# Kernel tuning notes

Measured on AMD Instinct MI355X. Metric: run time of the kernel, lower is better.

The kernel has to match this reference:

```python
import jax, jax.numpy as jnp
import numpy as np

B, T, D, H = 8, 4096, 1024, 1024


def log_g(x):
    # log of g(x) = relu(x)+0.5 for x>=0, sigmoid(x) for x<0 (continuous at 0)
    return jnp.where(x >= 0, jnp.log(jax.nn.relu(x) + 0.5), -jax.nn.softplus(-x))


def setup_inputs() -> dict:
    key = jax.random.key(0)
    k0, k1, k2, k3, k4, k5 = jax.random.split(key, 6)
    s = 1.0 / np.sqrt(D)
    return {
        "x": jax.random.normal(k0, (B, T, D), jnp.float32),
        "h_0": jax.random.normal(k1, (B, H), jnp.float32),
        "Wz": jax.random.uniform(k2, (H, D), jnp.float32, -s, s),
        "bz": jax.random.uniform(k3, (H,), jnp.float32, -s, s),
        "Wh": jax.random.uniform(k4, (H, D), jnp.float32, -s, s),
        "bh": jax.random.uniform(k5, (H,), jnp.float32, -s, s),
    }


def reference(x, h_0, Wz, bz, Wh, bh):
    # gate pre-activation k: (B,T,H)
    k = jnp.einsum("btd,hd->bth", x, Wz) + bz
    log_z = -jax.nn.softplus(-k)        # log sigmoid(k)
    log_coeffs = -jax.nn.softplus(k)    # log (1 - sigmoid(k))
    log_h_0 = log_g(h_0)[:, None, :]    # (B,1,H)
    log_tilde_h = log_g(jnp.einsum("btd,hd->bth", x, Wh) + bh)
    log_values = jnp.concatenate([log_h_0, log_z + log_tilde_h], axis=1)  # (B,T+1,H)
    # parallel scan in log space
    a_star = jnp.pad(jnp.cumsum(log_coeffs, axis=1), ((0, 0), (1, 0), (0, 0)))
    log_h = a_star + jax.lax.cumlogsumexp(log_values - a_star, axis=1)
    h = jnp.exp(log_h)                  # (B,T+1,H)
    return h[:, -T:, :]
```

## Files before the change

kernel.cpp:

```cpp
#include <hip/hip_runtime.h>
#include <hip/hip_bf16.h>

#define Bb 8
#define Tt 4096
#define Dd 1024
#define Hh 1024
#define Mm (Bb * Tt)
#define NCHUNK 32
#define CLEN 128

typedef float f32x4 __attribute__((ext_vector_type(4)));
typedef short bf16x8 __attribute__((ext_vector_type(8)));

__device__ __forceinline__ unsigned f2bfu(float x) {
  unsigned u = __float_as_uint(x);
  return (u + 0x7fffu + ((u >> 16) & 1u)) >> 16;
}
__device__ __forceinline__ float bflo(unsigned u) { return __uint_as_float(u << 16); }
__device__ __forceinline__ float bfhi(unsigned u) { return __uint_as_float(u & 0xffff0000u); }

__global__ void cvt_kernel(const float* __restrict__ src, unsigned short* __restrict__ dst,
                           int n4) {
  int i = blockIdx.x * blockDim.x + threadIdx.x;
  int stride = gridDim.x * blockDim.x;
  for (; i < n4; i += stride) {
    float4 v = reinterpret_cast<const float4*>(src)[i];
    ushort4 o;
    o.x = (unsigned short)f2bfu(v.x);
    o.y = (unsigned short)f2bfu(v.y);
    o.z = (unsigned short)f2bfu(v.z);
    o.w = (unsigned short)f2bfu(v.w);
    reinterpret_cast<ushort4*>(dst)[i] = o;
  }
}

__device__ __forceinline__ void async16(const unsigned short* g, unsigned short* l) {
  __builtin_amdgcn_global_load_lds(
      (const __attribute__((address_space(1))) unsigned int*)g,
      (__attribute__((address_space(3))) unsigned int*)l, 16, 0, 0);
}

__global__ void __launch_bounds__(256, 2) gemm_kernel(
    const unsigned short* __restrict__ xb,
    const unsigned short* __restrict__ wzb,
    const unsigned short* __restrict__ whb,
    const float* __restrict__ bz,
    const float* __restrict__ bh,
    unsigned int* __restrict__ P) {
  __shared__ unsigned short As[128 * 64];
  __shared__ unsigned short Bs[128 * 64];
  const int m0 = blockIdx.x * 128;
  const int h0 = blockIdx.y * 64;
  const int t = threadIdx.x;
  const int w = t >> 6;
  const int l = t & 63;
  const int ln = l & 15;
  const int l4 = l >> 4;

  f32x4 acc[2][8];
#pragma unroll
  for (int mf = 0; mf < 2; ++mf)
#pragma unroll
    for (int nf = 0; nf < 8; ++nf)
      acc[mf][nf] = f32x4{0.f, 0.f, 0.f, 0.f};

  for (int kt = 0; kt < Dd / 64; ++kt) {
    const int k0 = kt * 64;
#pragma unroll
    for (int i = 0; i < 4; ++i) {
      const int blk = i * 256 + t;
      const int r = blk >> 3;
      const int slot = (blk & 7) ^ (r & 7);
      async16(xb + (size_t)(m0 + r) * Dd + (k0 + slot * 8), &As[blk * 8]);
    }
#pragma unroll
    for (int i = 0; i < 4; ++i) {
      const int blk = i * 256 + t;
      const int r = blk >> 3;
      const int slot = (blk & 7) ^ (r & 7);
      const unsigned short* src =
          (r < 64) ? (wzb + (size_t)(h0 + r) * Dd + (k0 + slot * 8))
                   : (whb + (size_t)(h0 + r - 64) * Dd + (k0 + slot * 8));
      async16(src, &Bs[blk * 8]);
    }
    __syncthreads();

#pragma unroll
    for (int kk = 0; kk < 2; ++kk) {
      bf16x8 af[2];
#pragma unroll
      for (int mf = 0; mf < 2; ++mf) {
        const int row = w * 32 + mf * 16 + ln;
        const int kb = (kk * 64 + l4 * 16) ^ ((row & 7) << 4);
        af[mf] = *reinterpret_cast<const bf16x8*>(
            reinterpret_cast<const char*>(As) + row * 128 + kb);
      }
#pragma unroll
      for (int nf = 0; nf < 8; ++nf) {
        const int row = nf * 16 + ln;
        const int kb = (kk * 64 + l4 * 16) ^ ((row & 7) << 4);
        bf16x8 bfr = *reinterpret_cast<const bf16x8*>(
            reinterpret_cast<const char*>(Bs) + row * 128 + kb);
#pragma unroll
        for (int mf = 0; mf < 2; ++mf)
          acc[mf][nf] =
              __builtin_amdgcn_mfma_f32_16x16x32_bf16(af[mf], bfr, acc[mf][nf], 0, 0, 0);
      }
    }
    __syncthreads();
  }

#pragma unroll
  for (int mf = 0; mf < 2; ++mf) {
#pragma unroll
    for (int nf = 0; nf < 4; ++nf) {
      const int hcol = h0 + nf * 16 + ln;
      const float bzv = bz[hcol];
      const float bhv = bh[hcol];
#pragma unroll
      for (int q = 0; q < 4; ++q) {
        const int m = m0 + w * 32 + mf * 16 + l4 * 4 + q;
        const float kv = acc[mf][nf][q] + bzv;
        const float pv = acc[mf][nf + 4][q] + bhv;
        const float ek = __expf(kv);
        const float a = 1.f / (1.f + ek);
        const float z = 1.f - a;
        const float g = (pv >= 0.f) ? (pv + 0.5f) : (1.f / (1.f + __expf(-pv)));
        const float c = z * g;
        P[(size_t)m * Hh + hcol] = f2bfu(a) | (f2bfu(c) << 16);
      }
    }
  }
}

__global__ void scan_pass1(const unsigned int* __restrict__ P,
                           float* __restrict__ Pp, float* __restrict__ Qq) {
  const int h = blockIdx.x * 256 + threadIdx.x;
  const int ch = blockIdx.y;
  const int b = blockIdx.z;
  const unsigned int* p = P + ((size_t)(b * Tt + ch * CLEN)) * Hh + h;
  float A = 1.f, Q = 0.f;
#pragma unroll 8
  for (int i = 0; i < CLEN; ++i) {
    const unsigned u = p[(size_t)i * Hh];
    Q = fmaf(bflo(u), Q, bfhi(u));
    A *= bflo(u);
  }
  const int idx = ch * (Bb * Hh) + b * Hh + h;
  Pp[idx] = A;
  Qq[idx] = Q;
}

__global__ void scan_pass2(const float* __restrict__ h0raw,
                           const float* __restrict__ Pp, const float* __restrict__ Qq,
                           float* __restrict__ Hinit) {
  const int bh = blockIdx.x * 256 + threadIdx.x;
  const float x = h0raw[bh];
  float hs = (x >= 0.f) ? (x + 0.5f) : (1.f / (1.f + __expf(-x)));
  for (int ch = 0; ch < NCHUNK; ++ch) {
    const int idx = ch * (Bb * Hh) + bh;
    Hinit[idx] = hs;
    hs = fmaf(Pp[idx], hs, Qq[idx]);
  }
}

__global__ void scan_pass3(const unsigned int* __restrict__ P,
                           const float* __restrict__ Hinit,
                           float* __restrict__ out) {
  const int h = blockIdx.x * 256 + threadIdx.x;
  const int ch = blockIdx.y;
  const int b = blockIdx.z;
  float hs = Hinit[ch * (Bb * Hh) + b * Hh + h];
  const size_t base = ((size_t)(b * Tt + ch * CLEN)) * Hh + h;
  const unsigned int* p = P + base;
  float* o = out + base;
#pragma unroll 8
  for (int i = 0; i < CLEN; ++i) {
    const unsigned u = p[(size_t)i * Hh];
    hs = fmaf(bflo(u), hs, bfhi(u));
    o[(size_t)i * Hh] = hs;
  }
}

extern "C" void kernel_launch(void* const* d_in, const int* in_sizes, int n_in,
                              void* d_out, int out_size, void* d_ws, size_t ws_size,
                              hipStream_t stream) {
  const float* x  = (const float*)d_in[0];
  const float* h0 = (const float*)d_in[1];
  const float* Wz = (const float*)d_in[2];
  const float* bz = (const float*)d_in[3];
  const float* Wh = (const float*)d_in[4];
  const float* bh = (const float*)d_in[5];
  float* out = (float*)d_out;

  char* ws = (char*)d_ws;
  unsigned short* xb  = (unsigned short*)(ws);
  unsigned short* wzb = (unsigned short*)(ws + 67108864);
  unsigned short* whb = (unsigned short*)(ws + 69206016);
  unsigned int*   P   = (unsigned int*)(ws + 71303168);
  float* Pp    = (float*)(ws + 205520896);
  float* Qq    = (float*)(ws + 206569472);
  float* Hinit = (float*)(ws + 207618048);

  cvt_kernel<<<4096, 256, 0, stream>>>(x, xb, Mm * Dd / 4);
  cvt_kernel<<<1024, 256, 0, stream>>>(Wz, wzb, Hh * Dd / 4);
  cvt_kernel<<<1024, 256, 0, stream>>>(Wh, whb, Hh * Dd / 4);

  dim3 ggrid(Mm / 128, Hh / 64);
  gemm_kernel<<<ggrid, 256, 0, stream>>>(xb, wzb, whb, bz, bh, P);

  dim3 sgrid(Hh / 256, NCHUNK, Bb);
  scan_pass1<<<sgrid, 256, 0, stream>>>(P, Pp, Qq);
  scan_pass2<<<Bb * Hh / 256, 256, 0, stream>>>(h0, Pp, Qq, Hinit);
  scan_pass3<<<sgrid, 256, 0, stream>>>(P, Hinit, out);
}
```

Measured before the change: 280.5 us.

## Rewrite GEMM as 256x128 tile with double-buffered async LDS pipeline

Replaces the 128x64 single-buffered GEMM with a 512-thread, 256x(64 Wz + 64 Wh interleaved) tile kernel. Global-to-LDS loads are double-buffered across K steps and interleaved with MFMA phases, using explicit vmcnt waits, barriers and setprio. It also adds a block-ID swizzle for L2 locality and a rotated LDS layout to avoid bank conflicts. The aim is to hide load latency and raise MFMA utilisation, at the cost of higher register and LDS pressure (128KB LDS, one block per CU) and hand-tuned synchronisation that could be fragile.

New measurement: 273.0 us. 2.7% less time.

```diff
diff --git a/kernel.cpp b/kernel.cpp
--- a/kernel.cpp
+++ b/kernel.cpp
@@ -40,88 +40,202 @@
       (__attribute__((address_space(3))) unsigned int*)l, 16, 0, 0);
 }
 
-__global__ void __launch_bounds__(256, 2) gemm_kernel(
+template <int MF0>
+__device__ __forceinline__ void mfma16(const bf16x8 af[4], const bf16x8 bfr[4],
+                                       f32x4 (&acc)[8][4]) {
+#pragma unroll
+  for (int i = 0; i < 4; ++i)
+#pragma unroll
+    for (int j = 0; j < 4; ++j)
+      acc[MF0 + i][j] =
+          __builtin_amdgcn_mfma_f32_16x16x32_bf16(af[i], bfr[j], acc[MF0 + i][j], 0, 0, 0);
+}
+
+__device__ __forceinline__ void phase_pre(bool guard) {
+  if (guard) asm volatile("s_waitcnt vmcnt(6)" ::: "memory");
+  __builtin_amdgcn_sched_barrier(0);
+  __builtin_amdgcn_s_barrier();
+}
+__device__ __forceinline__ void phase_post() {
+  __builtin_amdgcn_sched_barrier(0);
+  __builtin_amdgcn_s_barrier();
+}
+
+__global__ void __launch_bounds__(512, 1) gemm_kernel(
     const unsigned short* __restrict__ xb,
     const unsigned short* __restrict__ wzb,
     const unsigned short* __restrict__ whb,
     const float* __restrict__ bz,
     const float* __restrict__ bh,
     unsigned int* __restrict__ P) {
-  __shared__ unsigned short As[128 * 64];
-  __shared__ unsigned short Bs[128 * 64];
-  const int m0 = blockIdx.x * 128;
-  const int h0 = blockIdx.y * 64;
-  const int t = threadIdx.x;
-  const int w = t >> 6;
-  const int l = t & 63;
-  const int ln = l & 15;
-  const int l4 = l >> 4;
-
-  f32x4 acc[2][8];
-#pragma unroll
-  for (int mf = 0; mf < 2; ++mf)
-#pragma unroll
-    for (int nf = 0; nf < 8; ++nf)
-      acc[mf][nf] = f32x4{0.f, 0.f, 0.f, 0.f};
-
-  for (int kt = 0; kt < Dd / 64; ++kt) {
-    const int k0 = kt * 64;
-#pragma unroll
-    for (int i = 0; i < 4; ++i) {
-      const int blk = i * 256 + t;
-      const int r = blk >> 3;
-      const int slot = (blk & 7) ^ (r & 7);
-      async16(xb + (size_t)(m0 + r) * Dd + (k0 + slot * 8), &As[blk * 8]);
-    }
-#pragma unroll
-    for (int i = 0; i < 4; ++i) {
-      const int blk = i * 256 + t;
-      const int r = blk >> 3;
-      const int slot = (blk & 7) ^ (r & 7);
-      const unsigned short* src =
-          (r < 64) ? (wzb + (size_t)(h0 + r) * Dd + (k0 + slot * 8))
-                   : (whb + (size_t)(h0 + r - 64) * Dd + (k0 + slot * 8));
-      async16(src, &Bs[blk * 8]);
-    }
-    __syncthreads();
-
-#pragma unroll
-    for (int kk = 0; kk < 2; ++kk) {
-      bf16x8 af[2];
-#pragma unroll
-      for (int mf = 0; mf < 2; ++mf) {
-        const int row = w * 32 + mf * 16 + ln;
-        const int kb = (kk * 64 + l4 * 16) ^ ((row & 7) << 4);
-        af[mf] = *reinterpret_cast<const bf16x8*>(
-            reinterpret_cast<const char*>(As) + row * 128 + kb);
-      }
-#pragma unroll
-      for (int nf = 0; nf < 8; ++nf) {
-        const int row = nf * 16 + ln;
-        const int kb = (kk * 64 + l4 * 16) ^ ((row & 7) << 4);
-        bf16x8 bfr = *reinterpret_cast<const bf16x8*>(
-            reinterpret_cast<const char*>(Bs) + row * 128 + kb);
-#pragma unroll
-        for (int mf = 0; mf < 2; ++mf)
-          acc[mf][nf] =
-              __builtin_amdgcn_mfma_f32_16x16x32_bf16(af[mf], bfr, acc[mf][nf], 0, 0, 0);
-      }
-    }
-    __syncthreads();
-  }
-
-#pragma unroll
-  for (int mf = 0; mf < 2; ++mf) {
-#pragma unroll
-    for (int nf = 0; nf < 4; ++nf) {
-      const int hcol = h0 + nf * 16 + ln;
-      const float bzv = bz[hcol];
-      const float bhv = bh[hcol];
+  __shared__ unsigned short lds[65536];
+  const int tid = threadIdx.x;
+  const int wid = tid >> 6;
+  const int wm = wid >> 2;
+  const int wn = wid & 3;
+  const int l = tid & 63, ln = l & 15, l4 = l >> 4;
+
+  const int id = blockIdx.x;
+  const int sw = (id & 7) * 128 + (id >> 3);
+  const int mb = sw >> 3, nb = sw & 7;
+  const int m0 = mb * 256, h0 = nb * 128;
+
+  auto stage_a = [&](int kt, int kh) {
+    unsigned short* dst = &lds[((kt & 1) * 2 + kh) * 8192];
+#pragma unroll
+    for (int c = 0; c < 2; ++c) {
+      const int blk = c * 512 + tid;
+      const int r = blk >> 2, sl = blk & 3;
+      const int chunk = (sl - (r >> 1)) & 3;
+      async16(xb + (size_t)(m0 + r) * Dd + (kt * 64 + kh * 32 + chunk * 8), dst + blk * 8);
+    }
+  };
+  auto stage_b = [&](int kt, int kh) {
+    unsigned short* dst = &lds[32768 + ((kt & 1) * 2 + kh) * 8192];
+#pragma unroll
+    for (int c = 0; c < 2; ++c) {
+      const int blk = c * 512 + tid;
+      const int r = blk >> 2, sl = blk & 3;
+      const int chunk = (sl - (r >> 1)) & 3;
+      const int sub16 = r >> 4;
+      const int hrow = h0 + ((sub16 >> 1) << 4) + (r & 15);
+      const unsigned short* src = (sub16 & 1) ? whb : wzb;
+      async16(src + (size_t)hrow * Dd + (kt * 64 + kh * 32 + chunk * 8), dst + blk * 8);
+    }
+  };
+
+  int oA[8], oB[4];
+#pragma unroll
+  for (int mf = 0; mf < 8; ++mf) {
+    const int row = wm * 128 + mf * 16 + ln;
+    const int sl = (l4 + (row >> 1)) & 3;
+    oA[mf] = row * 32 + sl * 8;
+  }
+#pragma unroll
+  for (int nf = 0; nf < 4; ++nf) {
+    const int row = wn * 64 + nf * 16 + ln;
+    const int sl = (l4 + (row >> 1)) & 3;
+    oB[nf] = row * 32 + sl * 8;
+  }
+
+  f32x4 acc[8][4];
+#pragma unroll
+  for (int i = 0; i < 8; ++i)
+#pragma unroll
+    for (int j = 0; j < 4; ++j) acc[i][j] = f32x4{0.f, 0.f, 0.f, 0.f};
+
+  stage_a(0, 0); stage_b(0, 0);
+  stage_a(0, 1); stage_b(0, 1);
+  stage_a(1, 0); stage_b(1, 0);
+  asm volatile("s_waitcnt vmcnt(8)" ::: "memory");
+  __builtin_amdgcn_sched_barrier(0);
+  __builtin_amdgcn_s_barrier();
+
+  for (int it = 0; it < 8; ++it) {
+    const int t1 = 2 * it + 1;
+    const int t2 = (2 * it + 2) & 15;
+    const int t3 = (2 * it + 3) & 15;
+    bf16x8 bfr[4];
+
+#define DS_B(SLOT, KH)                                                        \
+  {                                                                           \
+    const unsigned short* base_ = &lds[32768 + ((SLOT)*2 + (KH)) * 8192];     \
+    bfr[0] = *(const bf16x8*)(base_ + oB[0]);                                 \
+    bfr[1] = *(const bf16x8*)(base_ + oB[1]);                                 \
+    bfr[2] = *(const bf16x8*)(base_ + oB[2]);                                 \
+    bfr[3] = *(const bf16x8*)(base_ + oB[3]);                                 \
+  }
+#define DS_A(SLOT, KH, MF0)                                                   \
+  {                                                                           \
+    const unsigned short* base_ = &lds[((SLOT)*2 + (KH)) * 8192];             \
+    af[0] = *(const bf16x8*)(base_ + oA[(MF0) + 0]);                          \
+    af[1] = *(const bf16x8*)(base_ + oA[(MF0) + 1]);                          \
+    af[2] = *(const bf16x8*)(base_ + oA[(MF0) + 2]);                          \
+    af[3] = *(const bf16x8*)(base_ + oA[(MF0) + 3]);                          \
+  }
+
+    {
+      bf16x8 af[4];
+      DS_B(0, 0); DS_A(0, 0, 0);
+      stage_a(t1, 1);
+      phase_pre(false);
+      __builtin_amdgcn_s_setprio(1); mfma16<0>(af, bfr, acc); __builtin_amdgcn_s_setprio(0);
+      phase_post();
+    }
+    {
+      bf16x8 af[4];
+      DS_A(0, 0, 4);
+      stage_b(t1, 1);
+      phase_pre(true);
+      __builtin_amdgcn_s_setprio(1); mfma16<4>(af, bfr, acc); __builtin_amdgcn_s_setprio(0);
+      phase_post();
+    }
+    {
+      bf16x8 af[4];
+      DS_B(0, 1); DS_A(0, 1, 0);
+      stage_a(t2, 0);
+      phase_pre(false);
+      __builtin_amdgcn_s_setprio(1); mfma16<0>(af, bfr, acc); __builtin_amdgcn_s_setprio(0);
+      phase_post();
+    }
+    {
+      bf16x8 af[4];
+      DS_A(0, 1, 4);
+      stage_b(t2, 0);
+      phase_pre(true);
+      __builtin_amdgcn_s_setprio(1); mfma16<4>(af, bfr, acc); __builtin_amdgcn_s_setprio(0);
+      phase_post();
+    }
+    {
+      bf16x8 af[4];
+      DS_B(1, 0); DS_A(1, 0, 0);
+      stage_a(t2, 1);
+      phase_pre(false);
+      __builtin_amdgcn_s_setprio(1); mfma16<0>(af, bfr, acc); __builtin_amdgcn_s_setprio(0);
+      phase_post();
+    }
+    {
+      bf16x8 af[4];
+      DS_A(1, 0, 4);
+      stage_b(t2, 1);
+      phase_pre(true);
+      __builtin_amdgcn_s_setprio(1); mfma16<4>(af, bfr, acc); __builtin_amdgcn_s_setprio(0);
+      phase_post();
+    }
+    {
+      bf16x8 af[4];
+      DS_B(1, 1); DS_A(1, 1, 0);
+      stage_a(t3, 0);
+      phase_pre(false);
+      __builtin_amdgcn_s_setprio(1); mfma16<0>(af, bfr, acc); __builtin_amdgcn_s_setprio(0);
+      phase_post();
+    }
+    {
+      bf16x8 af[4];
+      DS_A(1, 1, 4);
+      stage_b(t3, 0);
+      phase_pre(true);
+      __builtin_amdgcn_s_setprio(1); mfma16<4>(af, bfr, acc); __builtin_amdgcn_s_setprio(0);
+      phase_post();
+    }
+#undef DS_A
+#undef DS_B
+  }
+
+  asm volatile("s_waitcnt vmcnt(0)" ::: "memory");
+
+#pragma unroll
+  for (int p = 0; p < 2; ++p) {
+    const int hcol = h0 + (wn * 2 + p) * 16 + ln;
+    const float bzv = bz[hcol];
+    const float bhv = bh[hcol];
+#pragma unroll
+    for (int mf = 0; mf < 8; ++mf) {
 #pragma unroll
       for (int q = 0; q < 4; ++q) {
-        const int m = m0 + w * 32 + mf * 16 + l4 * 4 + q;
-        const float kv = acc[mf][nf][q] + bzv;
-        const float pv = acc[mf][nf + 4][q] + bhv;
+        const int m = m0 + wm * 128 + mf * 16 + l4 * 4 + q;
+        const float kv = acc[mf][2 * p][q] + bzv;
+        const float pv = acc[mf][2 * p + 1][q] + bhv;
         const float ek = __expf(kv);
         const float a = 1.f / (1.f + ek);
         const float z = 1.f - a;
@@ -206,8 +320,7 @@
   cvt_kernel<<<1024, 256, 0, stream>>>(Wz, wzb, Hh * Dd / 4);
   cvt_kernel<<<1024, 256, 0, stream>>>(Wh, whb, Hh * Dd / 4);
 
-  dim3 ggrid(Mm / 128, Hh / 64);
-  gemm_kernel<<<ggrid, 256, 0, stream>>>(xb, wzb, whb, bz, bh, P);
+  gemm_kernel<<<1024, 512, 0, stream>>>(xb, wzb, whb, bz, bh, P);
 
   dim3 sgrid(Hh / 256, NCHUNK, Bb);
   scan_pass1<<<sgrid, 256, 0, stream>>>(P, Pp, Qq);
```

## Rewrite GEMM as 256x128 tile with 4-stage async LDS pipeline

Applied to the files above, without the earlier changes.

The fused gate/value GEMM becomes a 512-thread, 256x128 output tile per block. It uses a 4-stage ring of 32-wide K slices loaded with async global-to-LDS copies, interleaved barriers, and s_setprio around the MFMA bursts. It also swizzles the block index for L2 locality and interleaves the Wz/Wh rows so each wave holds matching k/p fragments. The aim is to hide memory latency and raise MFMA density compared with the previous single-buffered 128x64 kernel, at the cost of more registers and a single block per CU.

Result: faster. 273.2 us (-2.6%).

```diff
diff --git a/kernel.cpp b/kernel.cpp
--- a/kernel.cpp
+++ b/kernel.cpp
@@ -40,88 +40,145 @@
       (__attribute__((address_space(3))) unsigned int*)l, 16, 0, 0);
 }
 
-__global__ void __launch_bounds__(256, 2) gemm_kernel(
+template <int MF0>
+__device__ __forceinline__ void mfma16(const bf16x8 af[4], const bf16x8 bfr[4],
+                                       f32x4 (&acc)[8][4]) {
+#pragma unroll
+  for (int i = 0; i < 4; ++i)
+#pragma unroll
+    for (int j = 0; j < 4; ++j)
+      acc[MF0 + i][j] =
+          __builtin_amdgcn_mfma_f32_16x16x32_bf16(af[i], bfr[j], acc[MF0 + i][j], 0, 0, 0);
+}
+
+__global__ void __launch_bounds__(512, 1) gemm_kernel(
     const unsigned short* __restrict__ xb,
     const unsigned short* __restrict__ wzb,
     const unsigned short* __restrict__ whb,
     const float* __restrict__ bz,
     const float* __restrict__ bh,
     unsigned int* __restrict__ P) {
-  __shared__ unsigned short As[128 * 64];
-  __shared__ unsigned short Bs[128 * 64];
-  const int m0 = blockIdx.x * 128;
-  const int h0 = blockIdx.y * 64;
-  const int t = threadIdx.x;
-  const int w = t >> 6;
-  const int l = t & 63;
-  const int ln = l & 15;
-  const int l4 = l >> 4;
-
-  f32x4 acc[2][8];
-#pragma unroll
-  for (int mf = 0; mf < 2; ++mf)
-#pragma unroll
-    for (int nf = 0; nf < 8; ++nf)
-      acc[mf][nf] = f32x4{0.f, 0.f, 0.f, 0.f};
-
-  for (int kt = 0; kt < Dd / 64; ++kt) {
-    const int k0 = kt * 64;
-#pragma unroll
-    for (int i = 0; i < 4; ++i) {
-      const int blk = i * 256 + t;
-      const int r = blk >> 3;
-      const int slot = (blk & 7) ^ (r & 7);
-      async16(xb + (size_t)(m0 + r) * Dd + (k0 + slot * 8), &As[blk * 8]);
-    }
-#pragma unroll
-    for (int i = 0; i < 4; ++i) {
-      const int blk = i * 256 + t;
-      const int r = blk >> 3;
-      const int slot = (blk & 7) ^ (r & 7);
-      const unsigned short* src =
-          (r < 64) ? (wzb + (size_t)(h0 + r) * Dd + (k0 + slot * 8))
-                   : (whb + (size_t)(h0 + r - 64) * Dd + (k0 + slot * 8));
-      async16(src, &Bs[blk * 8]);
-    }
-    __syncthreads();
-
-#pragma unroll
-    for (int kk = 0; kk < 2; ++kk) {
-      bf16x8 af[2];
-#pragma unroll
-      for (int mf = 0; mf < 2; ++mf) {
-        const int row = w * 32 + mf * 16 + ln;
-        const int kb = (kk * 64 + l4 * 16) ^ ((row & 7) << 4);
-        af[mf] = *reinterpret_cast<const bf16x8*>(
-            reinterpret_cast<const char*>(As) + row * 128 + kb);
-      }
-#pragma unroll
-      for (int nf = 0; nf < 8; ++nf) {
-        const int row = nf * 16 + ln;
-        const int kb = (kk * 64 + l4 * 16) ^ ((row & 7) << 4);
-        bf16x8 bfr = *reinterpret_cast<const bf16x8*>(
-            reinterpret_cast<const char*>(Bs) + row * 128 + kb);
-#pragma unroll
-        for (int mf = 0; mf < 2; ++mf)
-          acc[mf][nf] =
-              __builtin_amdgcn_mfma_f32_16x16x32_bf16(af[mf], bfr, acc[mf][nf], 0, 0, 0);
-      }
-    }
-    __syncthreads();
-  }
-
-#pragma unroll
-  for (int mf = 0; mf < 2; ++mf) {
-#pragma unroll
-    for (int nf = 0; nf < 4; ++nf) {
-      const int hcol = h0 + nf * 16 + ln;
-      const float bzv = bz[hcol];
-      const float bhv = bh[hcol];
+  __shared__ unsigned short lds[65536];
+  const int tid = threadIdx.x;
+  const int wid = tid >> 6;
+  const int wm = wid >> 2;
+  const int wn = wid & 3;
+  const int l = tid & 63, ln = l & 15, l4 = l >> 4;
+
+  const int id = blockIdx.x;
+  const int sw = (id & 7) * 128 + (id >> 3);
+  const int mb = sw >> 3, nb = sw & 7;
+  const int m0 = mb * 256, h0 = nb * 128;
+
+  const int r0 = tid >> 2;
+  const int chunk = ((tid & 3) - (tid >> 3)) & 3;
+  const unsigned short* agp = xb + (size_t)(m0 + r0) * Dd + chunk * 8;
+  const int sub16 = r0 >> 4;
+  const int hrow0 = h0 + ((sub16 >> 1) << 4) + (r0 & 15);
+  const unsigned short* bgp =
+      ((sub16 & 1) ? whb : wzb) + (size_t)hrow0 * Dd + chunk * 8;
+  const int dstoff = tid * 8;
+
+  auto stA = [&](int reg) {
+    unsigned short* d = &lds[reg * 8192] + dstoff;
+    async16(agp, d);
+    async16(agp + (size_t)128 * Dd, d + 4096);
+    agp += 32;
+  };
+  auto stB = [&](int reg) {
+    unsigned short* d = &lds[32768 + reg * 8192] + dstoff;
+    async16(bgp, d);
+    async16(bgp + (size_t)64 * Dd, d + 4096);
+    bgp += 32;
+  };
+
+  int oA[8], oB[4];
+#pragma unroll
+  for (int mf = 0; mf < 8; ++mf) {
+    const int row = wm * 128 + mf * 16 + ln;
+    const int sl = (l4 + (row >> 1)) & 3;
+    oA[mf] = row * 32 + sl * 8;
+  }
+#pragma unroll
+  for (int nf = 0; nf < 4; ++nf) {
+    const int row = wn * 64 + nf * 16 + ln;
+    const int sl = (l4 + (row >> 1)) & 3;
+    oB[nf] = row * 32 + sl * 8;
+  }
+
+  f32x4 acc[8][4];
+#pragma unroll
+  for (int i = 0; i < 8; ++i)
+#pragma unroll
+    for (int j = 0; j < 4; ++j) acc[i][j] = f32x4{0.f, 0.f, 0.f, 0.f};
+
+  stA(0); stB(0);
+  stA(1); stB(1);
+  stA(2); stB(2);
+  asm volatile("s_waitcnt vmcnt(4)" ::: "memory");
+  __builtin_amdgcn_s_barrier();
+
+#define PAIR(P, G)                                                        \
+  {                                                                       \
+    bf16x8 bfr[4];                                                        \
+    const unsigned short* ba = &lds[(P) * 8192];                          \
+    const unsigned short* bb = &lds[32768 + (P) * 8192];                  \
+    bfr[0] = *(const bf16x8*)(bb + oB[0]);                                \
+    bfr[1] = *(const bf16x8*)(bb + oB[1]);                                \
+    bfr[2] = *(const bf16x8*)(bb + oB[2]);                                \
+    bfr[3] = *(const bf16x8*)(bb + oB[3]);                                \
+    {                                                                     \
+      bf16x8 af[4];                                                       \
+      af[0] = *(const bf16x8*)(ba + oA[0]);                               \
+      af[1] = *(const bf16x8*)(ba + oA[1]);                               \
+      af[2] = *(const bf16x8*)(ba + oA[2]);                               \
+      af[3] = *(const bf16x8*)(ba + oA[3]);                               \
+      stA(((P) + 3) & 3);                                                 \
+      __builtin_amdgcn_s_barrier();                                       \
+      __builtin_amdgcn_s_setprio(1);                                      \
+      mfma16<0>(af, bfr, acc);                                            \
+      __builtin_amdgcn_s_setprio(0);                                      \
+      __builtin_amdgcn_s_barrier();                                       \
+    }                                                                     \
+    {                                                                     \
+      bf16x8 af[4];                                                       \
+      af[0] = *(const bf16x8*)(ba + oA[4]);                               \
+      af[1] = *(const bf16x8*)(ba + oA[5]);                               \
+      af[2] = *(const bf16x8*)(ba + oA[6]);                               \
+      af[3] = *(const bf16x8*)(ba + oA[7]);                               \
+      stB(((P) + 3) & 3);                                                 \
+      __builtin_amdgcn_s_barrier();                                       \
+      __builtin_amdgcn_s_setprio(1);                                      \
+      mfma16<4>(af, bfr, acc);                                            \
+      __builtin_amdgcn_s_setprio(0);                                      \
+      if (G) asm volatile("s_waitcnt vmcnt(4)" ::: "memory");             \
+      __builtin_amdgcn_s_barrier();                                       \
+    }                                                                     \
+  }
+
+#pragma unroll 1
+  for (int it = 0; it < 8; ++it) {
+    PAIR(0, 0)
+    PAIR(1, 1)
+    PAIR(2, 0)
+    PAIR(3, 1)
+  }
+#undef PAIR
+
+  asm volatile("s_waitcnt vmcnt(0)" ::: "memory");
+
+#pragma unroll
+  for (int p = 0; p < 2; ++p) {
+    const int hcol = h0 + (wn * 2 + p) * 16 + ln;
+    const float bzv = bz[hcol];
+    const float bhv = bh[hcol];
+#pragma unroll
+    for (int mf = 0; mf < 8; ++mf) {
 #pragma unroll
       for (int q = 0; q < 4; ++q) {
-        const int m = m0 + w * 32 + mf * 16 + l4 * 4 + q;
-        const float kv = acc[mf][nf][q] + bzv;
-        const float pv = acc[mf][nf + 4][q] + bhv;
+        const int m = m0 + wm * 128 + mf * 16 + l4 * 4 + q;
+        const float kv = acc[mf][2 * p][q] + bzv;
+        const float pv = acc[mf][2 * p + 1][q] + bhv;
         const float ek = __expf(kv);
         const float a = 1.f / (1.f + ek);
         const float z = 1.f - a;
@@ -206,8 +263,7 @@
   cvt_kernel<<<1024, 256, 0, stream>>>(Wz, wzb, Hh * Dd / 4);
   cvt_kernel<<<1024, 256, 0, stream>>>(Wh, whb, Hh * Dd / 4);
 
-  dim3 ggrid(Mm / 128, Hh / 64);
-  gemm_kernel<<<ggrid, 256, 0, stream>>>(xb, wzb, whb, bz, bh, P);
+  gemm_kernel<<<1024, 512, 0, stream>>>(xb, wzb, whb, bz, bh, P);
 
   dim3 sgrid(Hh / 256, NCHUNK, Bb);
   scan_pass1<<<sgrid, 256, 0, stream>>>(P, Pp, Qq);
```
